# Optimization experiments

Hardware: AMD Instinct MI355X
Metric: run time of the kernel (lower is better)

Reference implementation:

```python
import jax, jax.numpy as jnp
import numpy as np

MARGIN = 0.2
ALMOST_INF = 9999.9


def _cdist(a, b):
    # Euclidean pairwise distances [N, M] via gram trick (matches torch.cdist p=2)
    d2 = (jnp.sum(a * a, axis=1)[:, None]
          + jnp.sum(b * b, axis=1)[None, :]
          - 2.0 * (a @ b.T))
    return jnp.sqrt(jnp.maximum(d2, 1e-12))


def setup_inputs() -> dict:
    key = jax.random.key(0)
    k1, k2, k3, k4 = jax.random.split(key, 4)
    N, D = 8192, 256
    return {
        "anchor": jax.random.normal(k1, (N, D), dtype=jnp.float32),
        "positive": jax.random.normal(k2, (N, D), dtype=jnp.float32),
        "negative": jax.random.normal(k3, (N, D), dtype=jnp.float32),
        "targets": jax.random.randint(k4, (N,), 0, 64, dtype=jnp.int64),
    }


def reference(anchor, positive, negative, targets):
    anchor_pos_dists = _cdist(anchor, positive)  # [N, N]
    anchor_neg_dists = _cdist(anchor, negative)  # [N, N]
    pos_mask = (targets[:, None] == targets[None, :]).astype(anchor.dtype)
    # hardest positive: max same-class distance per anchor
    max_pos = jnp.max(anchor_pos_dists * pos_mask, axis=1)
    # hardest negative: min distance per anchor, same-class entries pushed to +inf-ish
    min_neg = jnp.min(anchor_neg_dists + ALMOST_INF * pos_mask, axis=1)
    losses = jax.nn.relu(max_pos - min_neg + MARGIN)
    return jnp.mean(losses)  # size_average=True
```

## Files before the change

### kernel.cpp

```cpp
#include <hip/hip_runtime.h>
#include <hip/hip_bf16.h>

typedef unsigned short u16;
typedef __bf16 bf16x8 __attribute__((ext_vector_type(8)));
typedef float f32x4 __attribute__((ext_vector_type(4)));

#define MARGIN 0.2f
#define NEG_INF -3.0e38f

__device__ __forceinline__ u16 f2bf_rne(float f) {
  unsigned u = __builtin_bit_cast(unsigned, f);
  u += 0x7FFFu + ((u >> 16) & 1u);
  return (u16)(u >> 16);
}

__global__ void prep_kernel(const float* __restrict__ A, const float* __restrict__ P,
                            const float* __restrict__ Ng, const int* __restrict__ tg,
                            u16* __restrict__ Ab, u16* __restrict__ Pb, u16* __restrict__ Nb,
                            float* __restrict__ an, float* __restrict__ pn, float* __restrict__ nn,
                            int* __restrict__ cls, float* __restrict__ out, int D, int N) {
  if (blockIdx.y == 0) {
    if (blockIdx.x == 0 && threadIdx.x == 0) out[0] = 0.f;
    if ((int)blockIdx.x < (N >> 8)) {
      const int i = blockIdx.x * 256 + threadIdx.x;
      cls[i] = tg[i];
    }
  }
  const int row  = blockIdx.x * 4 + (threadIdx.x >> 6);
  const int lane = threadIdx.x & 63;
  const float* src; u16* dst; float* nrm;
  if (blockIdx.y == 0)      { src = A;  dst = Ab; nrm = an; }
  else if (blockIdx.y == 1) { src = P;  dst = Pb; nrm = pn; }
  else                      { src = Ng; dst = Nb; nrm = nn; }
  float4 v = *(const float4*)(src + (size_t)row * D + lane * 4);
  float ss = v.x * v.x + v.y * v.y + v.z * v.z + v.w * v.w;
  ushort4 o = make_ushort4(f2bf_rne(v.x), f2bf_rne(v.y), f2bf_rne(v.z), f2bf_rne(v.w));
  *(ushort4*)(dst + (size_t)row * D + lane * 4) = o;
  #pragma unroll
  for (int m = 1; m < 64; m <<= 1) ss += __shfl_xor(ss, m);
  if (lane == 0) nrm[row] = ss;
}

__device__ __forceinline__ void stage_tile(const u16* __restrict__ g, u16* lds,
                                           int rbase, int kb, int D, int w, int l) {
  #pragma unroll
  for (int c = 0; c < 4; ++c) {
    const int row  = w * 32 + c * 8 + (l >> 3);
    const int slot = (l & 7) ^ (row & 7);
    const u16* gp = g + (size_t)(rbase + row) * D + kb * 64 + slot * 8;
    u16* lp = lds + w * 2048 + c * 512;
    __builtin_amdgcn_global_load_lds((const __attribute__((address_space(1))) void*)gp,
                                     (__attribute__((address_space(3))) void*)lp,
                                     16, 0, 0);
  }
}

__global__ __launch_bounds__(256, 4) void triplet_tile_kernel(
    const u16* __restrict__ Ab, const u16* __restrict__ Pb, const u16* __restrict__ Nb,
    const float* __restrict__ pnorm, const float* __restrict__ nnorm,
    const int* __restrict__ cls,
    float* __restrict__ maxP, float* __restrict__ minN, int N, int D, int nCB) {
  __shared__ __align__(16) u16 As[128 * 64];
  __shared__ __align__(16) u16 Bs[128 * 64];
  __shared__ float nS[128];
  __shared__ int   ccS[128], rcS[128];
  __shared__ float red[2][128];

  const int cb = blockIdx.x, rb = blockIdx.y, z = blockIdx.z;
  const int rowbase = rb * 128, colbase = cb * 128;
  const u16*  __restrict__ Bmat = z ? Nb : Pb;
  const float* __restrict__ cn  = z ? nnorm : pnorm;
  const float sgn = z ? -1.f : 1.f;

  const int t = threadIdx.x, l = t & 63, w = t >> 6;
  const int wr = w >> 1, wc = w & 1, g = l >> 4, lr = l & 15;

  if (t < 128) {
    nS[t]  = cn[colbase + t];
    ccS[t] = cls[colbase + t];
  } else {
    rcS[t - 128] = cls[rowbase + (t - 128)];
  }

  const int swz   = ((l >> 4) ^ (l & 7)) * 16;
  const int abase = (wr * 64 + lr) * 128 + swz;
  const int bbase = (wc * 64 + lr) * 128 + swz;
  const char* __restrict__ Ac = (const char*)As;
  const char* __restrict__ Bc = (const char*)Bs;

  f32x4 acc[4][4];
  #pragma unroll
  for (int m = 0; m < 4; ++m)
    #pragma unroll
    for (int n = 0; n < 4; ++n) acc[m][n] = (f32x4){0.f, 0.f, 0.f, 0.f};

  const int nKB = D / 64;
  for (int kb = 0; kb < nKB; ++kb) {
    __syncthreads();
    stage_tile(Ab,   As, rowbase, kb, D, w, l);
    stage_tile(Bmat, Bs, colbase, kb, D, w, l);
    __syncthreads();
    #pragma unroll
    for (int kk = 0; kk < 2; ++kk) {
      const int sel = kk * 64;
      bf16x8 af[4], bf[4];
      #pragma unroll
      for (int m = 0; m < 4; ++m)
        af[m] = *(const bf16x8*)(Ac + ((abase ^ sel) + m * 2048));
      #pragma unroll
      for (int n = 0; n < 4; ++n)
        bf[n] = *(const bf16x8*)(Bc + ((bbase ^ sel) + n * 2048));
      #pragma unroll
      for (int m = 0; m < 4; ++m)
        #pragma unroll
        for (int n = 0; n < 4; ++n)
          acc[m][n] = __builtin_amdgcn_mfma_f32_16x16x32_bf16(af[m], bf[n], acc[m][n], 0, 0, 0);
    }
  }

  #pragma unroll
  for (int m = 0; m < 4; ++m) {
    #pragma unroll
    for (int r = 0; r < 4; ++r) {
      const int row = wr * 64 + m * 16 + g * 4 + r;
      const int rc  = rcS[row];
      float v = NEG_INF;
      #pragma unroll
      for (int n = 0; n < 4; ++n) {
        const int col = wc * 64 + n * 16 + lr;
        const bool same = (rc == ccS[col]);
        const bool want = z ? !same : same;
        const float q = sgn * fmaf(-2.f, acc[m][n][r], nS[col]);
        v = want ? fmaxf(v, q) : v;
      }
      #pragma unroll
      for (int msk = 1; msk < 16; msk <<= 1) v = fmaxf(v, __shfl_xor(v, msk));
      if (lr == 0) red[wc][row] = v;
    }
  }
  __syncthreads();
  if (t < 128) {
    const float v = fmaxf(red[0][t], red[1][t]);
    float* __restrict__ outp = z ? minN : maxP;
    outp[(size_t)(rowbase + t) * nCB + cb] = sgn * v;
  }
}

__global__ void finalize_kernel(const float* __restrict__ maxP, const float* __restrict__ minN,
                                const float* __restrict__ an, float* out, int N, int nCB) {
  const int r = blockIdx.x * 256 + threadIdx.x;
  const float4* __restrict__ mp = (const float4*)(maxP + (size_t)r * nCB);
  const float4* __restrict__ np = (const float4*)(minN + (size_t)r * nCB);
  float mx = NEG_INF, mn = 3.0e38f;
  for (int i = 0; i < (nCB >> 2); ++i) {
    const float4 a = mp[i];
    mx = fmaxf(mx, fmaxf(fmaxf(a.x, a.y), fmaxf(a.z, a.w)));
    const float4 b = np[i];
    mn = fminf(mn, fminf(fminf(b.x, b.y), fminf(b.z, b.w)));
  }
  const float aa = an[r];
  const float dp = sqrtf(fmaxf(aa + mx, 1e-12f));
  const float dn = sqrtf(fmaxf(aa + mn, 1e-12f));
  float loss = fmaxf(dp - dn + MARGIN, 0.f);
  #pragma unroll
  for (int msk = 1; msk < 64; msk <<= 1) loss += __shfl_xor(loss, msk);
  __shared__ float s[4];
  if ((threadIdx.x & 63) == 0) s[threadIdx.x >> 6] = loss;
  __syncthreads();
  if (threadIdx.x == 0)
    atomicAdd(out, (s[0] + s[1] + s[2] + s[3]) * (1.0f / N));
}

extern "C" void kernel_launch(void* const* d_in, const int* in_sizes, int n_in,
                              void* d_out, int out_size, void* d_ws, size_t ws_size,
                              hipStream_t stream) {
  const float* A  = (const float*)d_in[0];
  const float* P  = (const float*)d_in[1];
  const float* Ng = (const float*)d_in[2];
  const int*   tg = (const int*)d_in[3];
  float* out = (float*)d_out;

  const int N = in_sizes[3];
  const int D = in_sizes[0] / N;
  const int nRB = N / 128, nCB = N / 128;

  char* ws = (char*)d_ws;
  const size_t bf = (size_t)N * D * sizeof(u16);
  u16* Ab = (u16*)ws;
  u16* Pb = (u16*)(ws + bf);
  u16* Nb = (u16*)(ws + 2 * bf);
  char* p = ws + 3 * bf;
  float* an = (float*)p; p += (size_t)N * 4;
  float* pn = (float*)p; p += (size_t)N * 4;
  float* nn = (float*)p; p += (size_t)N * 4;
  int*  cls = (int*)p;   p += (size_t)N * 4;
  float* maxP = (float*)p; p += (size_t)nCB * N * 4;
  float* minN = (float*)p;

  prep_kernel<<<dim3(N / 4, 3), 256, 0, stream>>>(A, P, Ng, tg, Ab, Pb, Nb,
                                                  an, pn, nn, cls, out, D, N);
  triplet_tile_kernel<<<dim3(nCB, nRB, 2), 256, 0, stream>>>(Ab, Pb, Nb, pn, nn, cls,
                                                             maxP, minN, N, D, nCB);
  finalize_kernel<<<N / 256, 256, 0, stream>>>(maxP, minN, an, out, N, nCB);
}
```

Baseline: 176.9 us.

## Keep anchor rows in registers and sweep 1024 columns per block

The main tile kernel is restructured so each block holds 128 anchor rows' full-K bf16 fragments in registers. It loops over 16 column tiles of 64 within a 1024-column group, staging only B tiles (full K=256) into LDS. This removes repeated A staging and shrinks the partial-result buffer from N/128 to N/1024 entries per row, so finalize does less work. In exchange it uses more registers (occupancy hint drops to 3), the grid is smaller, and there is no double buffering of B loads.

```diff
diff --git a/kernel.cpp b/kernel.cpp
--- a/kernel.cpp
+++ b/kernel.cpp
@@ -4,6 +4,7 @@
 typedef unsigned short u16;
 typedef __bf16 bf16x8 __attribute__((ext_vector_type(8)));
 typedef float f32x4 __attribute__((ext_vector_type(4)));
+typedef int   i32x4 __attribute__((ext_vector_type(4)));
 
 #define MARGIN 0.2f
 #define NEG_INF -3.0e38f
@@ -41,122 +42,120 @@
   if (lane == 0) nrm[row] = ss;
 }
 
-__device__ __forceinline__ void stage_tile(const u16* __restrict__ g, u16* lds,
-                                           int rbase, int kb, int D, int w, int l) {
-  #pragma unroll
-  for (int c = 0; c < 4; ++c) {
-    const int row  = w * 32 + c * 8 + (l >> 3);
-    const int slot = (l & 7) ^ (row & 7);
-    const u16* gp = g + (size_t)(rbase + row) * D + kb * 64 + slot * 8;
-    u16* lp = lds + w * 2048 + c * 512;
-    __builtin_amdgcn_global_load_lds((const __attribute__((address_space(1))) void*)gp,
-                                     (__attribute__((address_space(3))) void*)lp,
-                                     16, 0, 0);
-  }
-}
-
-__global__ __launch_bounds__(256, 4) void triplet_tile_kernel(
+__global__ __launch_bounds__(256, 3) void triplet_cb_kernel(
     const u16* __restrict__ Ab, const u16* __restrict__ Pb, const u16* __restrict__ Nb,
     const float* __restrict__ pnorm, const float* __restrict__ nnorm,
     const int* __restrict__ cls,
-    float* __restrict__ maxP, float* __restrict__ minN, int N, int D, int nCB) {
-  __shared__ __align__(16) u16 As[128 * 64];
-  __shared__ __align__(16) u16 Bs[128 * 64];
-  __shared__ float nS[128];
-  __shared__ int   ccS[128], rcS[128];
-  __shared__ float red[2][128];
-
-  const int cb = blockIdx.x, rb = blockIdx.y, z = blockIdx.z;
-  const int rowbase = rb * 128, colbase = cb * 128;
+    float* __restrict__ maxP, float* __restrict__ minN, int N, int D, int ngrp) {
+  __shared__ __align__(16) u16  Bs[64 * 256];
+  __shared__ __align__(16) int   ccL[1024];
+  __shared__ __align__(16) float snL[1024];
+
+  const int grp = blockIdx.x, rg_ = blockIdx.y, z = blockIdx.z;
+  const int rowbase = rg_ * 128, colbase0 = grp * 1024;
   const u16*  __restrict__ Bmat = z ? Nb : Pb;
   const float* __restrict__ cn  = z ? nnorm : pnorm;
-  const float sgn = z ? -1.f : 1.f;
+  const float sgn  = z ? -1.f : 1.f;
+  const float coef = -2.f * sgn;
 
   const int t = threadIdx.x, l = t & 63, w = t >> 6;
-  const int wr = w >> 1, wc = w & 1, g = l >> 4, lr = l & 15;
-
-  if (t < 128) {
-    nS[t]  = cn[colbase + t];
-    ccS[t] = cls[colbase + t];
-  } else {
-    rcS[t - 128] = cls[rowbase + (t - 128)];
-  }
-
-  const int swz   = ((l >> 4) ^ (l & 7)) * 16;
-  const int abase = (wr * 64 + lr) * 128 + swz;
-  const int bbase = (wc * 64 + lr) * 128 + swz;
-  const char* __restrict__ Ac = (const char*)As;
-  const char* __restrict__ Bc = (const char*)Bs;
-
-  f32x4 acc[4][4];
-  #pragma unroll
-  for (int m = 0; m < 4; ++m)
-    #pragma unroll
-    for (int n = 0; n < 4; ++n) acc[m][n] = (f32x4){0.f, 0.f, 0.f, 0.f};
-
-  const int nKB = D / 64;
-  for (int kb = 0; kb < nKB; ++kb) {
+  const int lr = l & 15, g = (l >> 4) & 3;
+
+  #pragma unroll
+  for (int i = 0; i < 4; ++i) {
+    const int c = i * 256 + t;
+    ccL[c] = cls[colbase0 + c];
+    snL[c] = sgn * cn[colbase0 + c];
+  }
+
+  const int arow0 = rowbase + w * 32 + lr;
+  bf16x8 af[2][8];
+  #pragma unroll
+  for (int rj = 0; rj < 2; ++rj)
+    #pragma unroll
+    for (int kk = 0; kk < 8; ++kk)
+      af[rj][kk] = *(const bf16x8*)(Ab + (size_t)(arow0 + rj * 16) * D + kk * 32 + g * 8);
+
+  int rc[2];
+  rc[0] = cls[arow0];
+  rc[1] = cls[arow0 + 16];
+
+  float vmax[2] = {NEG_INF, NEG_INF};
+
+  const int rowpar = w * 2 + (l >> 5);
+  const int slot0  = l & 31;
+
+  for (int cb = 0; cb < 16; ++cb) {
+    const int colbase = colbase0 + cb * 64;
     __syncthreads();
-    stage_tile(Ab,   As, rowbase, kb, D, w, l);
-    stage_tile(Bmat, Bs, colbase, kb, D, w, l);
+    #pragma unroll
+    for (int c = 0; c < 8; ++c) {
+      const int row  = c * 8 + rowpar;
+      const int slot = slot0 ^ (row & 7);
+      const u16* gp = Bmat + (size_t)(colbase + row) * D + slot * 8;
+      u16* lp = Bs + c * 2048 + w * 512;
+      __builtin_amdgcn_global_load_lds((const __attribute__((address_space(1))) void*)gp,
+                                       (__attribute__((address_space(3))) void*)lp,
+                                       16, 0, 0);
+    }
     __syncthreads();
-    #pragma unroll
-    for (int kk = 0; kk < 2; ++kk) {
-      const int sel = kk * 64;
-      bf16x8 af[4], bf[4];
+
+    f32x4 acc[4][2];
+    const f32x4 zero = (f32x4){0.f, 0.f, 0.f, 0.f};
+    #pragma unroll
+    for (int kk = 0; kk < 8; ++kk) {
+      bf16x8 bf[4];
       #pragma unroll
-      for (int m = 0; m < 4; ++m)
-        af[m] = *(const bf16x8*)(Ac + ((abase ^ sel) + m * 2048));
-      #pragma unroll
-      for (int n = 0; n < 4; ++n)
-        bf[n] = *(const bf16x8*)(Bc + ((bbase ^ sel) + n * 2048));
-      #pragma unroll
-      for (int m = 0; m < 4; ++m)
-        #pragma unroll
-        for (int n = 0; n < 4; ++n)
-          acc[m][n] = __builtin_amdgcn_mfma_f32_16x16x32_bf16(af[m], bf[n], acc[m][n], 0, 0, 0);
-    }
-  }
-
-  #pragma unroll
-  for (int m = 0; m < 4; ++m) {
-    #pragma unroll
-    for (int r = 0; r < 4; ++r) {
-      const int row = wr * 64 + m * 16 + g * 4 + r;
-      const int rc  = rcS[row];
-      float v = NEG_INF;
-      #pragma unroll
-      for (int n = 0; n < 4; ++n) {
-        const int col = wc * 64 + n * 16 + lr;
-        const bool same = (rc == ccS[col]);
-        const bool want = z ? !same : same;
-        const float q = sgn * fmaf(-2.f, acc[m][n][r], nS[col]);
-        v = want ? fmaxf(v, q) : v;
+      for (int ci = 0; ci < 4; ++ci) {
+        const int p    = ci * 16 + lr;
+        const int addr = p * 512 + (((kk * 4 + g) ^ (l & 7)) * 16);
+        bf[ci] = *(const bf16x8*)((const char*)Bs + addr);
       }
       #pragma unroll
-      for (int msk = 1; msk < 16; msk <<= 1) v = fmaxf(v, __shfl_xor(v, msk));
-      if (lr == 0) red[wc][row] = v;
-    }
-  }
-  __syncthreads();
-  if (t < 128) {
-    const float v = fmaxf(red[0][t], red[1][t]);
-    float* __restrict__ outp = z ? minN : maxP;
-    outp[(size_t)(rowbase + t) * nCB + cb] = sgn * v;
+      for (int ci = 0; ci < 4; ++ci)
+        #pragma unroll
+        for (int rj = 0; rj < 2; ++rj)
+          acc[ci][rj] = __builtin_amdgcn_mfma_f32_16x16x32_bf16(
+              bf[ci], af[rj][kk], kk == 0 ? zero : acc[ci][rj], 0, 0, 0);
+    }
+
+    #pragma unroll
+    for (int ci = 0; ci < 4; ++ci) {
+      const int cl = cb * 64 + ci * 16 + g * 4;
+      const i32x4 cc4 = *(const i32x4*)&ccL[cl];
+      const f32x4 sn4 = *(const f32x4*)&snL[cl];
+      #pragma unroll
+      for (int rg = 0; rg < 4; ++rg)
+        #pragma unroll
+        for (int rj = 0; rj < 2; ++rj) {
+          const float q   = fmaf(coef, acc[ci][rj][rg], sn4[rg]);
+          const bool same = (rc[rj] == cc4[rg]);
+          const bool want = z ? !same : same;
+          vmax[rj] = fmaxf(vmax[rj], want ? q : NEG_INF);
+        }
+    }
+  }
+
+  #pragma unroll
+  for (int rj = 0; rj < 2; ++rj) {
+    float v = vmax[rj];
+    v = fmaxf(v, __shfl_xor(v, 16));
+    v = fmaxf(v, __shfl_xor(v, 32));
+    if ((l >> 4) == 0) {
+      const int row = arow0 + rj * 16;
+      float* __restrict__ outp = z ? minN : maxP;
+      outp[(size_t)row * ngrp + grp] = sgn * v;
+    }
   }
 }
 
 __global__ void finalize_kernel(const float* __restrict__ maxP, const float* __restrict__ minN,
-                                const float* __restrict__ an, float* out, int N, int nCB) {
+                                const float* __restrict__ an, float* out, int N, int ngrp) {
   const int r = blockIdx.x * 256 + threadIdx.x;
-  const float4* __restrict__ mp = (const float4*)(maxP + (size_t)r * nCB);
-  const float4* __restrict__ np = (const float4*)(minN + (size_t)r * nCB);
   float mx = NEG_INF, mn = 3.0e38f;
-  for (int i = 0; i < (nCB >> 2); ++i) {
-    const float4 a = mp[i];
-    mx = fmaxf(mx, fmaxf(fmaxf(a.x, a.y), fmaxf(a.z, a.w)));
-    const float4 b = np[i];
-    mn = fminf(mn, fminf(fminf(b.x, b.y), fminf(b.z, b.w)));
+  for (int i = 0; i < ngrp; ++i) {
+    mx = fmaxf(mx, maxP[(size_t)r * ngrp + i]);
+    mn = fminf(mn, minN[(size_t)r * ngrp + i]);
   }
   const float aa = an[r];
   const float dp = sqrtf(fmaxf(aa + mx, 1e-12f));
@@ -182,7 +181,7 @@
 
   const int N = in_sizes[3];
   const int D = in_sizes[0] / N;
-  const int nRB = N / 128, nCB = N / 128;
+  const int ngrp = N / 1024;
 
   char* ws = (char*)d_ws;
   const size_t bf = (size_t)N * D * sizeof(u16);
@@ -194,12 +193,12 @@
   float* pn = (float*)p; p += (size_t)N * 4;
   float* nn = (float*)p; p += (size_t)N * 4;
   int*  cls = (int*)p;   p += (size_t)N * 4;
-  float* maxP = (float*)p; p += (size_t)nCB * N * 4;
+  float* maxP = (float*)p; p += (size_t)N * ngrp * 4;
   float* minN = (float*)p;
 
   prep_kernel<<<dim3(N / 4, 3), 256, 0, stream>>>(A, P, Ng, tg, Ab, Pb, Nb,
                                                   an, pn, nn, cls, out, D, N);
-  triplet_tile_kernel<<<dim3(nCB, nRB, 2), 256, 0, stream>>>(Ab, Pb, Nb, pn, nn, cls,
-                                                             maxP, minN, N, D, nCB);
-  finalize_kernel<<<N / 256, 256, 0, stream>>>(maxP, minN, an, out, N, nCB);
-}
+  triplet_cb_kernel<<<dim3(ngrp, N / 128, 2), 256, 0, stream>>>(Ab, Pb, Nb, pn, nn, cls,
+                                                                maxP, minN, N, D, ngrp);
+  finalize_kernel<<<N / 256, 256, 0, stream>>>(maxP, minN, an, out, N, ngrp);
+}
```

After: 149.2 us. -15.7%, faster.
